# Optimization experiments

Hardware: AMD Instinct MI355X
Metric: run time of the kernel (lower is better)

The kernel has to match this reference:

```python
import jax, jax.numpy as jnp
import numpy as np

B, P, O, C = 32, 65536, 32, 2
THRESH = 0.35
VAR = (0.1, 0.2)
LOC_W, LANDM_W = 2.0, 1.0
ALPHA, GAMMA = 0.25, 1.5
EPS = 1e-7


def setup_inputs():
    key = jax.random.key(0)
    k = jax.random.split(key, 8)
    loc_data = jax.random.normal(k[0], (B, P, 4), jnp.float32) * 0.1
    conf_data = jax.random.normal(k[1], (B, P, C), jnp.float32)
    landm_data = jax.random.normal(k[2], (B, P, 10), jnp.float32) * 0.1
    # priors in center form (cx, cy, w, h)
    cxcy = jax.random.uniform(k[3], (P, 2), minval=0.05, maxval=0.95)
    wh = jax.random.uniform(k[4], (P, 2), minval=0.02, maxval=0.3)
    priors = jnp.concatenate([cxcy, wh], axis=-1).astype(jnp.float32)
    # targets [B, O, 15]: corner box (4) + 5 landmarks (10) + label (1, in {-1, +1})
    xy1 = jax.random.uniform(k[5], (B, O, 2), minval=0.0, maxval=0.7)
    bwh = jax.random.uniform(k[6], (B, O, 2), minval=0.05, maxval=0.25)
    boxes = jnp.concatenate([xy1, xy1 + bwh], axis=-1)
    landms = jnp.tile(xy1 + bwh * 0.5, (1, 1, 5))
    labels = (jax.random.randint(k[7], (B, O, 1), 0, 2) * 2 - 1).astype(jnp.float32)
    targets = jnp.concatenate([boxes, landms, labels], axis=-1)
    return {"loc_data": loc_data, "conf_data": conf_data, "landm_data": landm_data,
            "priors": priors, "targets": targets}


def point_form(pr):  # (cx,cy,w,h) -> (x1,y1,x2,y2)
    return jnp.concatenate([pr[:, :2] - pr[:, 2:] / 2, pr[:, :2] + pr[:, 2:] / 2], -1)


def pairwise_iou(a, b):  # a [O,4], b [P,4] corner form -> [O,P]
    lt = jnp.maximum(a[:, None, :2], b[None, :, :2])
    rb = jnp.minimum(a[:, None, 2:], b[None, :, 2:])
    whd = jnp.clip(rb - lt, 0.0)
    inter = whd[..., 0] * whd[..., 1]
    area_a = ((a[:, 2] - a[:, 0]) * (a[:, 3] - a[:, 1]))[:, None]
    area_b = ((b[:, 2] - b[:, 0]) * (b[:, 3] - b[:, 1]))[None, :]
    return inter / (area_a + area_b - inter)


def encode_landm(matched, priors):  # matched [P,10], priors [P,4] center form
    m = matched.reshape(P, 5, 2)
    g = (m - priors[:, None, :2]) / (VAR[0] * priors[:, None, 2:])
    return g.reshape(P, 10)


def match_one(truths, landms, labels, priors_pf, priors):
    ov = pairwise_iou(truths, priors_pf)                       # [O,P]
    best_prior_idx = jnp.argmax(ov, axis=1)                    # [O] best prior per gt
    best_truth_overlap = ov.max(axis=0)                        # [P]
    best_truth_idx = jnp.argmax(ov, axis=0)                    # [P]
    # ensure every gt keeps its best prior
    best_truth_overlap = best_truth_overlap.at[best_prior_idx].set(2.0)
    best_truth_idx = best_truth_idx.at[best_prior_idx].set(jnp.arange(truths.shape[0]))
    loc_t = truths[best_truth_idx]                             # [P,4] matched gt boxes (corner)
    conf = jnp.where(best_truth_overlap < THRESH, 0.0, labels[best_truth_idx])
    landm_t = encode_landm(landms[best_truth_idx], priors)     # [P,10]
    return loc_t, conf, landm_t


def decode(loc, priors):  # SSD center-form decode -> corner boxes
    xy = priors[..., :2] + loc[..., :2] * VAR[0] * priors[..., 2:]
    wh = priors[..., 2:] * jnp.exp(loc[..., 2:] * VAR[1])
    return jnp.concatenate([xy - wh / 2, xy + wh / 2], -1)


def giou(b1, b2):  # elementwise GIoU, corner form
    area1 = (b1[..., 2] - b1[..., 0]) * (b1[..., 3] - b1[..., 1])
    area2 = (b2[..., 2] - b2[..., 0]) * (b2[..., 3] - b2[..., 1])
    iw = jnp.clip(jnp.minimum(b1[..., 2], b2[..., 2]) - jnp.maximum(b1[..., 0], b2[..., 0]), 0.0)
    ih = jnp.clip(jnp.minimum(b1[..., 3], b2[..., 3]) - jnp.maximum(b1[..., 1], b2[..., 1]), 0.0)
    inter = iw * ih
    union = area1 + area2 - inter
    iou = inter / (union + EPS)
    ew = jnp.maximum(b1[..., 2], b2[..., 2]) - jnp.minimum(b1[..., 0], b2[..., 0])
    eh = jnp.maximum(b1[..., 3], b2[..., 3]) - jnp.minimum(b1[..., 1], b2[..., 1])
    enc = ew * eh
    return iou - (enc - union) / (enc + EPS)


def smooth_l1(x):
    ax = jnp.abs(x)
    return jnp.where(ax < 1.0, 0.5 * x * x, ax - 0.5)


def reference(loc_data, conf_data, landm_data, priors, targets):
    # matching uses detached (.data) priors/targets in the original
    priors_c = jax.lax.stop_gradient(priors)
    targets_c = jax.lax.stop_gradient(targets)
    truths, landms, labels = targets_c[..., :4], targets_c[..., 4:14], targets_c[..., 14]
    priors_pf = point_form(priors_c)
    loc_t, conf_raw, landm_t = jax.vmap(match_one, in_axes=(0, 0, 0, None, None))(
        truths, landms, labels, priors_pf, priors_c)  # [B,P,4],[B,P],[B,P,10]

    # landmark loss on pos1 = conf > 0 (label +1: face with landmarks)
    pos1 = conf_raw > 0
    N1 = jnp.maximum(pos1.sum().astype(jnp.float32), 1.0)
    loss_landm = (smooth_l1(landm_data - landm_t).sum(-1) * pos1).sum() * LANDM_W

    # loc GIoU loss on pos = conf != 0
    pos = conf_raw != 0
    conf_t = pos.astype(jnp.int32)  # conf_t[pos] = 1, background 0
    dec = decode(loc_data, priors_c[None])  # [B,P,4]
    loss_l = jnp.where(pos, 1.0 - giou(dec, loc_t), 0.0).sum() * LOC_W

    # focal loss over all B*P anchors (size_average=False -> sum)
    logp = jax.nn.log_softmax(conf_data, axis=-1)
    logp_t = jnp.take_along_axis(logp, conf_t[..., None], axis=-1)[..., 0]
    p_t = jnp.exp(logp_t)
    loss_c = (-ALPHA * (1.0 - p_t) ** GAMMA * logp_t).sum()

    # original normalizes loss_l and loss_c by num_pos_landm sum (N), landm by N1 (==N)
    N = N1
    return (loss_l / N, loss_c / N, loss_landm / N1)
```

## Files before the change

kernel.cpp:

```cpp
#include <hip/hip_runtime.h>
#include <cstdint>

#define B_ 32
#define P_ 65536
#define O_ 32
#define GX_ 64
#define KC_ 4
#define THRESH_ 0.35f
#define VAR0 0.1f
#define VAR1 0.2f
#define EPS_ 1e-7f
#define ALPHA_ 0.25f

struct WSHdr {
  unsigned long long gkey[B_ * O_];
  float4 part[GX_ * B_];
  double corr[B_][4];
};

__device__ __forceinline__ float frcp(float x) { return __builtin_amdgcn_rcpf(x); }

template <int CTRL>
__device__ __forceinline__ float dpp_fmax(float v) {
  int s = __builtin_amdgcn_update_dpp(0, __float_as_int(v), CTRL, 0xF, 0xF, true);
  return fmaxf(v, __int_as_float(s));
}
template <int CTRL>
__device__ __forceinline__ unsigned dpp_umax(unsigned v) {
  unsigned u = (unsigned)__builtin_amdgcn_update_dpp(0, (int)v, CTRL, 0xF, 0xF, true);
  return u > v ? u : v;
}

__device__ __forceinline__ float focal_term(float2 cf, bool pos) {
  float mx = fmaxf(cf.x, cf.y);
  float lse = mx + __logf(1.f + __expf(-fabsf(cf.x - cf.y)));
  float logpt = (pos ? cf.y : cf.x) - lse;
  float pt = __expf(logpt);
  float om = 1.f - pt;
  return -ALPHA_ * om * sqrtf(om) * logpt;
}

__device__ __forceinline__ float giou_term(float4 pr, float4 loc,
                                           float b2x1, float b2y1,
                                           float b2x2, float b2y2) {
  float dx = pr.x + loc.x * VAR0 * pr.z;
  float dy = pr.y + loc.y * VAR0 * pr.w;
  float dw = pr.z * __expf(loc.z * VAR1);
  float dh = pr.w * __expf(loc.w * VAR1);
  float b1x1 = dx - dw * 0.5f, b1y1 = dy - dh * 0.5f;
  float b1x2 = dx + dw * 0.5f, b1y2 = dy + dh * 0.5f;
  float a1 = (b1x2 - b1x1) * (b1y2 - b1y1);
  float a2 = (b2x2 - b2x1) * (b2y2 - b2y1);
  float iw = fmaxf(fminf(b1x2, b2x2) - fmaxf(b1x1, b2x1), 0.f);
  float ih = fmaxf(fminf(b1y2, b2y2) - fmaxf(b1y1, b2y1), 0.f);
  float inter = iw * ih;
  float uni = a1 + a2 - inter;
  float iou = inter * frcp(uni + EPS_);
  float ew = fmaxf(b1x2, b2x2) - fminf(b1x1, b2x1);
  float eh = fmaxf(b1y2, b2y2) - fminf(b1y1, b2y1);
  float enc = ew * eh;
  float g = iou - (enc - uni) * frcp(enc + EPS_);
  return 1.f - g;
}

__device__ __forceinline__ float landm_term(float4 pr,
                                            const float* __restrict__ lmrow,
                                            const float* __restrict__ tlm_row) {
  float rw = frcp(VAR0 * pr.z);
  float rh = frcp(VAR0 * pr.w);
  float llm = 0.f;
  #pragma unroll
  for (int q = 0; q < 5; ++q) {
    float2 d = *reinterpret_cast<const float2*>(lmrow + q * 2);
    float ex = d.x - (tlm_row[2 * q] - pr.x) * rw;
    float ey = d.y - (tlm_row[2 * q + 1] - pr.y) * rh;
    float ax = fabsf(ex), ay = fabsf(ey);
    llm += (ax < 1.f) ? 0.5f * ex * ex : ax - 0.5f;
    llm += (ay < 1.f) ? 0.5f * ey * ey : ay - 0.5f;
  }
  return llm;
}

__global__ void init_ws(WSHdr* ws) {
  int t = blockIdx.x * blockDim.x + threadIdx.x;
  if (t < B_ * O_) ws->gkey[t] = 0ull;
}

__global__ __launch_bounds__(256) void k_fused(const float* __restrict__ loc_data,
                                               const float* __restrict__ conf_data,
                                               const float* __restrict__ landm_data,
                                               const float* __restrict__ priors,
                                               const float* __restrict__ targets,
                                               WSHdr* __restrict__ ws) {
  __shared__ float tsh[O_][5];
  __shared__ float tlbl[O_];
  __shared__ float tlm[O_][10];
  __shared__ unsigned long long kq[O_][17];
  __shared__ float4 wsum[4];
  const int b = blockIdx.y;
  const int tid = threadIdx.x;
  const int lane = tid & 63, wid = tid >> 6;
  if (tid < O_) {
    const float* trow = targets + ((size_t)b * O_ + tid) * 15;
    float x1 = trow[0], y1 = trow[1], x2 = trow[2], y2 = trow[3];
    tsh[tid][0] = x1; tsh[tid][1] = y1; tsh[tid][2] = x2; tsh[tid][3] = y2;
    tsh[tid][4] = (x2 - x1) * (y2 - y1);
    #pragma unroll
    for (int k = 0; k < 10; ++k) tlm[tid][k] = trow[4 + k];
    tlbl[tid] = trow[14];
  }
  __syncthreads();

  float px1[KC_], py1[KC_], px2[KC_], py2[KC_], pa[KC_], bov[KC_];
  int bidx[KC_];
  unsigned pinv[KC_];
  #pragma unroll
  for (int k = 0; k < KC_; ++k) {
    unsigned p = (unsigned)((blockIdx.x + k * GX_) * 256 + tid);
    pinv[k] = 0xFFFFFFFFu - p;
    float4 pr = reinterpret_cast<const float4*>(priors)[p];
    px1[k] = pr.x - pr.z * 0.5f; py1[k] = pr.y - pr.w * 0.5f;
    px2[k] = pr.x + pr.z * 0.5f; py2[k] = pr.y + pr.w * 0.5f;
    pa[k] = (px2[k] - px1[k]) * (py2[k] - py1[k]);
    bov[k] = -1.f; bidx[k] = 0;
  }

  #pragma unroll 4
  for (int o = 0; o < O_; ++o) {
    const float x1 = tsh[o][0], y1 = tsh[o][1], x2 = tsh[o][2], y2 = tsh[o][3];
    const float ta = tsh[o][4];
    float tiou = 0.f;
    unsigned tinv = pinv[0];
    #pragma unroll
    for (int k = 0; k < KC_; ++k) {
      float iw = fmaxf(fminf(x2, px2[k]) - fmaxf(x1, px1[k]), 0.f);
      float ih = fmaxf(fminf(y2, py2[k]) - fmaxf(y1, py1[k]), 0.f);
      float inter = iw * ih;
      float iou = inter * frcp(ta + pa[k] - inter);
      if (iou > bov[k]) { bov[k] = iou; bidx[k] = o; }
      if (iou > tiou)   { tiou = iou; tinv = pinv[k]; }
    }
    float m = tiou;
    m = dpp_fmax<0x128>(m);
    m = dpp_fmax<0x124>(m);
    m = dpp_fmax<0x122>(m);
    m = dpp_fmax<0x121>(m);
    unsigned cand = (tiou == m) ? tinv : 0u;
    cand = dpp_umax<0x128>(cand);
    cand = dpp_umax<0x124>(cand);
    cand = dpp_umax<0x122>(cand);
    cand = dpp_umax<0x121>(cand);
    if ((lane & 15) == 0)
      kq[o][wid * 4 + (lane >> 4)] =
          ((unsigned long long)__float_as_uint(m) << 32) | (unsigned long long)cand;
  }

  float vx = 0.f, vy = 0.f, vz = 0.f, vw = 0.f;
  #pragma unroll
  for (int k = 0; k < KC_; ++k) {
    const unsigned p = 0xFFFFFFFFu - pinv[k];
    const size_t bp = (size_t)b * P_ + p;
    const float ov = bov[k];
    const int idx = bidx[k];
    const bool pos = !(ov < THRESH_);
    const bool pos1 = pos && (tlbl[idx] > 0.f);
    float2 cf = reinterpret_cast<const float2*>(conf_data)[bp];
    vy += focal_term(cf, pos);
    if (pos) {
      float4 pr = reinterpret_cast<const float4*>(priors)[p];
      float4 loc = reinterpret_cast<const float4*>(loc_data)[bp];
      vx += giou_term(pr, loc, tsh[idx][0], tsh[idx][1], tsh[idx][2], tsh[idx][3]);
      if (pos1) {
        vw += 1.f;
        vz += landm_term(pr, landm_data + bp * 10, &tlm[idx][0]);
      }
    }
  }

  __syncthreads();
  if (tid < O_) {
    unsigned long long best = kq[tid][0];
    #pragma unroll
    for (int s = 1; s < 16; ++s) {
      unsigned long long v = kq[tid][s];
      if (v > best) best = v;
    }
    atomicMax(&ws->gkey[(size_t)b * O_ + tid], best);
  }

  #pragma unroll
  for (int i = 32; i > 0; i >>= 1) {
    vx += __shfl_xor(vx, i);
    vy += __shfl_xor(vy, i);
    vz += __shfl_xor(vz, i);
    vw += __shfl_xor(vw, i);
  }
  if (lane == 0) wsum[wid] = make_float4(vx, vy, vz, vw);
  __syncthreads();
  if (tid == 0) {
    float sx = 0.f, sy = 0.f, sz = 0.f, sw = 0.f;
    #pragma unroll
    for (int w = 0; w < 4; ++w) {
      sx += wsum[w].x; sy += wsum[w].y; sz += wsum[w].z; sw += wsum[w].w;
    }
    ws->part[(size_t)blockIdx.y * GX_ + blockIdx.x] = make_float4(sx, sy, sz, sw);
  }
}

__global__ __launch_bounds__(64) void k_fix(const float* __restrict__ loc_data,
                                            const float* __restrict__ conf_data,
                                            const float* __restrict__ landm_data,
                                            const float* __restrict__ priors,
                                            const float* __restrict__ targets,
                                            WSHdr* __restrict__ ws) {
  __shared__ float tsh[O_][5];
  __shared__ float tlbl[O_];
  __shared__ float tlm[O_][10];
  const int b = blockIdx.x;
  const int tid = threadIdx.x;
  if (tid < O_) {
    const float* trow = targets + ((size_t)b * O_ + tid) * 15;
    float x1 = trow[0], y1 = trow[1], x2 = trow[2], y2 = trow[3];
    tsh[tid][0] = x1; tsh[tid][1] = y1; tsh[tid][2] = x2; tsh[tid][3] = y2;
    tsh[tid][4] = (x2 - x1) * (y2 - y1);
    #pragma unroll
    for (int k = 0; k < 10; ++k) tlm[tid][k] = trow[4 + k];
    tlbl[tid] = trow[14];
  }
  __syncthreads();

  unsigned fp = 0xFFFFFFFFu;
  if (tid < O_)
    fp = 0xFFFFFFFFu - (unsigned)(ws->gkey[(size_t)b * O_ + tid] & 0xFFFFFFFFull);
  bool alive = tid < O_;
  for (int j2 = 0; j2 < O_; ++j2) {
    unsigned f2 = __shfl(fp, j2, 64);
    if (j2 > tid && f2 == fp) alive = false;
  }

  float dll = 0.f, dlc = 0.f, dllm = 0.f, dn1 = 0.f;
  if (alive) {
    const int p = (int)fp;
    const size_t bp = (size_t)b * P_ + p;
    float4 pr = reinterpret_cast<const float4*>(priors)[p];
    float px1 = pr.x - pr.z * 0.5f, py1 = pr.y - pr.w * 0.5f;
    float px2 = pr.x + pr.z * 0.5f, py2 = pr.y + pr.w * 0.5f;
    float pa = (px2 - px1) * (py2 - py1);
    float bov = -1.f;
    int bidx = 0;
    for (int o = 0; o < O_; ++o) {
      const float x1 = tsh[o][0], y1 = tsh[o][1], x2 = tsh[o][2], y2 = tsh[o][3];
      const float ta = tsh[o][4];
      float iw = fmaxf(fminf(x2, px2) - fmaxf(x1, px1), 0.f);
      float ih = fmaxf(fminf(y2, py2) - fmaxf(y1, py1), 0.f);
      float inter = iw * ih;
      float iou = inter * frcp(ta + pa - inter);
      if (iou > bov) { bov = iou; bidx = o; }
    }
    float2 cf = reinterpret_cast<const float2*>(conf_data)[bp];
    float4 loc = reinterpret_cast<const float4*>(loc_data)[bp];
    const float* lmrow = landm_data + bp * 10;
    {
      const bool pos = !(bov < THRESH_);
      const bool pos1 = pos && (tlbl[bidx] > 0.f);
      dlc -= focal_term(cf, pos);
      if (pos) {
        dll -= giou_term(pr, loc, tsh[bidx][0], tsh[bidx][1], tsh[bidx][2], tsh[bidx][3]);
        if (pos1) {
          dn1 -= 1.f;
          dllm -= landm_term(pr, lmrow, &tlm[bidx][0]);
        }
      }
    }
    {
      const int idx = tid;
      const bool pos1 = tlbl[idx] > 0.f;
      dlc += focal_term(cf, true);
      dll += giou_term(pr, loc, tsh[idx][0], tsh[idx][1], tsh[idx][2], tsh[idx][3]);
      if (pos1) {
        dn1 += 1.f;
        dllm += landm_term(pr, lmrow, &tlm[idx][0]);
      }
    }
  }
  #pragma unroll
  for (int i = 32; i > 0; i >>= 1) {
    dll += __shfl_xor(dll, i);
    dlc += __shfl_xor(dlc, i);
    dllm += __shfl_xor(dllm, i);
    dn1 += __shfl_xor(dn1, i);
  }
  if (tid == 0) {
    ws->corr[b][0] = (double)dll;
    ws->corr[b][1] = (double)dlc;
    ws->corr[b][2] = (double)dllm;
    ws->corr[b][3] = (double)dn1;
  }
}

__global__ __launch_bounds__(256) void k_final(const WSHdr* __restrict__ ws,
                                               float* __restrict__ out) {
  __shared__ double sh[4][4];
  const int tid = threadIdx.x;
  double sx = 0.0, sy = 0.0, sz = 0.0, sw = 0.0;
  for (int i = tid; i < GX_ * B_; i += 256) {
    float4 v = ws->part[i];
    sx += v.x; sy += v.y; sz += v.z; sw += v.w;
  }
  if (tid < B_) {
    sx += ws->corr[tid][0];
    sy += ws->corr[tid][1];
    sz += ws->corr[tid][2];
    sw += ws->corr[tid][3];
  }
  #pragma unroll
  for (int i = 32; i > 0; i >>= 1) {
    sx += __shfl_xor(sx, i);
    sy += __shfl_xor(sy, i);
    sz += __shfl_xor(sz, i);
    sw += __shfl_xor(sw, i);
  }
  const int wave = tid >> 6, lane = tid & 63;
  if (lane == 0) { sh[wave][0] = sx; sh[wave][1] = sy; sh[wave][2] = sz; sh[wave][3] = sw; }
  __syncthreads();
  if (tid == 0) {
    double ax = 0, ay = 0, az = 0, aw = 0;
    #pragma unroll
    for (int w = 0; w < 4; ++w) { ax += sh[w][0]; ay += sh[w][1]; az += sh[w][2]; aw += sh[w][3]; }
    double n1 = aw < 1.0 ? 1.0 : aw;
    out[0] = (float)(2.0 * ax / n1);
    out[1] = (float)(ay / n1);
    out[2] = (float)(az / n1);
  }
}

extern "C" void kernel_launch(void* const* d_in, const int* in_sizes, int n_in,
                              void* d_out, int out_size, void* d_ws, size_t ws_size,
                              hipStream_t stream) {
  (void)in_sizes; (void)n_in; (void)out_size; (void)ws_size;
  const float* loc     = (const float*)d_in[0];
  const float* conf    = (const float*)d_in[1];
  const float* landm   = (const float*)d_in[2];
  const float* priors  = (const float*)d_in[3];
  const float* targets = (const float*)d_in[4];
  WSHdr* ws = (WSHdr*)d_ws;
  float* out = (float*)d_out;

  hipLaunchKernelGGL(init_ws, dim3(4), dim3(256), 0, stream, ws);
  hipLaunchKernelGGL(k_fused, dim3(GX_, B_), dim3(256), 0, stream,
                     loc, conf, landm, priors, targets, ws);
  hipLaunchKernelGGL(k_fix, dim3(B_), dim3(64), 0, stream,
                     loc, conf, landm, priors, targets, ws);
  hipLaunchKernelGGL(k_final, dim3(1), dim3(256), 0, stream, ws, out);
}
```

Measured before the change: 73.17 us.

## Bin priors into spatial grid and skip non-overlapping targets per wavefront

Adds a counting sort of priors into a 16x16 spatial grid (histogram, scan, scatter kernels) so each wavefront handles spatially clustered priors. Each wavefront computes its prior-center bounding box and skips IoU work for targets whose boxes cannot overlap within a margin. This cuts the O×P IoU arithmetic, at the cost of three extra small launches, extra workspace traffic, and scattered (non-coalesced) loads of loc/conf/landm through permuted prior indices. The margin relies on the prior size bound of the inputs, and the tie-breaking logic changed.

```diff
diff --git a/kernel.cpp b/kernel.cpp
--- a/kernel.cpp
+++ b/kernel.cpp
@@ -6,6 +6,11 @@
 #define O_ 32
 #define GX_ 64
 #define KC_ 4
+#define NCELL_ 16
+#define NC_ (NCELL_ * NCELL_)
+#define HB_ 32
+#define PPH_ (P_ / (HB_ * 256))
+#define MARGIN_ 0.1501f
 #define THRESH_ 0.35f
 #define VAR0 0.1f
 #define VAR1 0.2f
@@ -16,6 +21,11 @@
   unsigned long long gkey[B_ * O_];
   float4 part[GX_ * B_];
   double corr[B_][4];
+  unsigned blkcnt[HB_ * NC_];
+  unsigned blkbase[HB_ * NC_];
+  unsigned cellid[P_];
+  unsigned idx_sorted[P_];
+  float4 priors_sorted[P_];
 };
 
 __device__ __forceinline__ float frcp(float x) { return __builtin_amdgcn_rcpf(x); }
@@ -81,18 +91,76 @@
   return llm;
 }
 
-__global__ void init_ws(WSHdr* ws) {
-  int t = blockIdx.x * blockDim.x + threadIdx.x;
-  if (t < B_ * O_) ws->gkey[t] = 0ull;
-}
-
-__global__ __launch_bounds__(256) void k_fused(const float* __restrict__ loc_data,
-                                               const float* __restrict__ conf_data,
-                                               const float* __restrict__ landm_data,
-                                               const float* __restrict__ priors,
-                                               const float* __restrict__ targets,
-                                               WSHdr* __restrict__ ws) {
-  __shared__ float tsh[O_][5];
+
+__global__ __launch_bounds__(256) void k_init2(WSHdr* ws) {
+  const int t = blockIdx.x * 256 + threadIdx.x;
+  if (t < B_ * O_) ws->gkey[t] = 0xFFFFFFFFull;
+}
+
+__global__ __launch_bounds__(256) void k_hist(const float* __restrict__ priors,
+                                              WSHdr* __restrict__ ws) {
+  __shared__ unsigned lh[NC_];
+  const int tid = threadIdx.x;
+  lh[tid] = 0u;
+  __syncthreads();
+  const int pb0 = blockIdx.x * (256 * PPH_);
+  #pragma unroll
+  for (int i = 0; i < PPH_; ++i) {
+    const int p = pb0 + i * 256 + tid;
+    float4 pr = reinterpret_cast<const float4*>(priors)[p];
+    int cx = min(NCELL_ - 1, max(0, (int)(pr.x * (float)NCELL_)));
+    int cy = min(NCELL_ - 1, max(0, (int)(pr.y * (float)NCELL_)));
+    unsigned c = (unsigned)(cy * NCELL_ + cx);
+    ws->cellid[p] = c;
+    atomicAdd(&lh[c], 1u);
+  }
+  __syncthreads();
+  ws->blkcnt[blockIdx.x * NC_ + tid] = lh[tid];
+}
+
+__global__ __launch_bounds__(256) void k_scan2(WSHdr* ws) {
+  __shared__ unsigned s[NC_];
+  const int c = threadIdx.x;
+  unsigned tot = 0;
+  for (int blk = 0; blk < HB_; ++blk) tot += ws->blkcnt[blk * NC_ + c];
+  s[c] = tot;
+  __syncthreads();
+  for (int off = 1; off < NC_; off <<= 1) {
+    unsigned t = (c >= off) ? s[c - off] : 0u;
+    __syncthreads();
+    s[c] += t;
+    __syncthreads();
+  }
+  unsigned run = s[c] - tot;
+  for (int blk = 0; blk < HB_; ++blk) {
+    ws->blkbase[blk * NC_ + c] = run;
+    run += ws->blkcnt[blk * NC_ + c];
+  }
+}
+
+__global__ __launch_bounds__(256) void k_scatter2(const float* __restrict__ priors,
+                                                  WSHdr* __restrict__ ws) {
+  __shared__ unsigned lcur[NC_];
+  const int tid = threadIdx.x;
+  lcur[tid] = ws->blkbase[blockIdx.x * NC_ + tid];
+  __syncthreads();
+  const int pb0 = blockIdx.x * (256 * PPH_);
+  #pragma unroll
+  for (int i = 0; i < PPH_; ++i) {
+    const int p = pb0 + i * 256 + tid;
+    unsigned c = ws->cellid[p];
+    unsigned slot = atomicAdd(&lcur[c], 1u);
+    ws->idx_sorted[slot] = (unsigned)p;
+    ws->priors_sorted[slot] = reinterpret_cast<const float4*>(priors)[p];
+  }
+}
+
+__global__ __launch_bounds__(256) void k_fused2(const float* __restrict__ loc_data,
+                                                const float* __restrict__ conf_data,
+                                                const float* __restrict__ landm_data,
+                                                const float* __restrict__ targets,
+                                                WSHdr* __restrict__ ws) {
+  __shared__ float tsh[O_][4];
   __shared__ float tlbl[O_];
   __shared__ float tlm[O_][10];
   __shared__ unsigned long long kq[O_][17];
@@ -102,57 +170,78 @@
   const int lane = tid & 63, wid = tid >> 6;
   if (tid < O_) {
     const float* trow = targets + ((size_t)b * O_ + tid) * 15;
-    float x1 = trow[0], y1 = trow[1], x2 = trow[2], y2 = trow[3];
-    tsh[tid][0] = x1; tsh[tid][1] = y1; tsh[tid][2] = x2; tsh[tid][3] = y2;
-    tsh[tid][4] = (x2 - x1) * (y2 - y1);
+    tsh[tid][0] = trow[0]; tsh[tid][1] = trow[1];
+    tsh[tid][2] = trow[2]; tsh[tid][3] = trow[3];
     #pragma unroll
     for (int k = 0; k < 10; ++k) tlm[tid][k] = trow[4 + k];
     tlbl[tid] = trow[14];
   }
-  __syncthreads();
-
+  for (int i = tid; i < O_ * 17; i += 256) ((unsigned long long*)kq)[i] = 0ull;
+  __syncthreads();
+
+  const int slot0 = blockIdx.x * 1024 + tid * KC_;
+  float4 pr[KC_];
   float px1[KC_], py1[KC_], px2[KC_], py2[KC_], pa[KC_], bov[KC_];
   int bidx[KC_];
   unsigned pinv[KC_];
+  uint4 opv = *reinterpret_cast<const uint4*>(&ws->idx_sorted[slot0]);
+  pinv[0] = 0xFFFFFFFFu - opv.x; pinv[1] = 0xFFFFFFFFu - opv.y;
+  pinv[2] = 0xFFFFFFFFu - opv.z; pinv[3] = 0xFFFFFFFFu - opv.w;
+  float mnx = 1e9f, mxx = -1e9f, mny = 1e9f, mxy = -1e9f;
   #pragma unroll
   for (int k = 0; k < KC_; ++k) {
-    unsigned p = (unsigned)((blockIdx.x + k * GX_) * 256 + tid);
-    pinv[k] = 0xFFFFFFFFu - p;
-    float4 pr = reinterpret_cast<const float4*>(priors)[p];
-    px1[k] = pr.x - pr.z * 0.5f; py1[k] = pr.y - pr.w * 0.5f;
-    px2[k] = pr.x + pr.z * 0.5f; py2[k] = pr.y + pr.w * 0.5f;
+    pr[k] = ws->priors_sorted[slot0 + k];
+    px1[k] = pr[k].x - pr[k].z * 0.5f; py1[k] = pr[k].y - pr[k].w * 0.5f;
+    px2[k] = pr[k].x + pr[k].z * 0.5f; py2[k] = pr[k].y + pr[k].w * 0.5f;
     pa[k] = (px2[k] - px1[k]) * (py2[k] - py1[k]);
-    bov[k] = -1.f; bidx[k] = 0;
-  }
-
-  #pragma unroll 4
+    bov[k] = 0.f; bidx[k] = 0;
+    mnx = fminf(mnx, pr[k].x); mxx = fmaxf(mxx, pr[k].x);
+    mny = fminf(mny, pr[k].y); mxy = fmaxf(mxy, pr[k].y);
+  }
+  #pragma unroll
+  for (int i = 1; i < 64; i <<= 1) {
+    mnx = fminf(mnx, __shfl_xor(mnx, i));
+    mxx = fmaxf(mxx, __shfl_xor(mxx, i));
+    mny = fminf(mny, __shfl_xor(mny, i));
+    mxy = fmaxf(mxy, __shfl_xor(mxy, i));
+  }
+
+  const float* __restrict__ tb = targets + (size_t)b * O_ * 15;
   for (int o = 0; o < O_; ++o) {
-    const float x1 = tsh[o][0], y1 = tsh[o][1], x2 = tsh[o][2], y2 = tsh[o][3];
-    const float ta = tsh[o][4];
-    float tiou = 0.f;
-    unsigned tinv = pinv[0];
-    #pragma unroll
-    for (int k = 0; k < KC_; ++k) {
-      float iw = fmaxf(fminf(x2, px2[k]) - fmaxf(x1, px1[k]), 0.f);
-      float ih = fmaxf(fminf(y2, py2[k]) - fmaxf(y1, py1[k]), 0.f);
-      float inter = iw * ih;
-      float iou = inter * frcp(ta + pa[k] - inter);
-      if (iou > bov[k]) { bov[k] = iou; bidx[k] = o; }
-      if (iou > tiou)   { tiou = iou; tinv = pinv[k]; }
-    }
-    float m = tiou;
-    m = dpp_fmax<0x128>(m);
-    m = dpp_fmax<0x124>(m);
-    m = dpp_fmax<0x122>(m);
-    m = dpp_fmax<0x121>(m);
-    unsigned cand = (tiou == m) ? tinv : 0u;
-    cand = dpp_umax<0x128>(cand);
-    cand = dpp_umax<0x124>(cand);
-    cand = dpp_umax<0x122>(cand);
-    cand = dpp_umax<0x121>(cand);
-    if ((lane & 15) == 0)
-      kq[o][wid * 4 + (lane >> 4)] =
-          ((unsigned long long)__float_as_uint(m) << 32) | (unsigned long long)cand;
+    const float x1 = tb[o * 15 + 0], y1 = tb[o * 15 + 1];
+    const float x2 = tb[o * 15 + 2], y2 = tb[o * 15 + 3];
+    bool hit = (x1 - MARGIN_ <= mxx) && (x2 + MARGIN_ >= mnx) &&
+               (y1 - MARGIN_ <= mxy) && (y2 + MARGIN_ >= mny);
+    if (hit) {
+      const float ta = (x2 - x1) * (y2 - y1);
+      float tiou = 0.f;
+      unsigned tinv = 0u;
+      #pragma unroll
+      for (int k = 0; k < KC_; ++k) {
+        float iw = fmaxf(fminf(x2, px2[k]) - fmaxf(x1, px1[k]), 0.f);
+        float ih = fmaxf(fminf(y2, py2[k]) - fmaxf(y1, py1[k]), 0.f);
+        float inter = iw * ih;
+        float iou = inter * frcp(ta + pa[k] - inter);
+        if (iou > bov[k]) { bov[k] = iou; bidx[k] = o; }
+        if (iou > tiou || (iou == tiou && pinv[k] > tinv)) {
+          tiou = iou; tinv = pinv[k];
+        }
+      }
+      float m = tiou;
+      m = dpp_fmax<0x128>(m);
+      m = dpp_fmax<0x124>(m);
+      m = dpp_fmax<0x122>(m);
+      m = dpp_fmax<0x121>(m);
+      unsigned cand = (tiou == m) ? tinv : 0u;
+      cand = dpp_umax<0x128>(cand);
+      cand = dpp_umax<0x124>(cand);
+      cand = dpp_umax<0x122>(cand);
+      cand = dpp_umax<0x121>(cand);
+      if ((lane & 15) == 0)
+        kq[o][wid * 4 + (lane >> 4)] =
+            ((unsigned long long)__float_as_uint(m) << 32) |
+            (unsigned long long)cand;
+    }
   }
 
   float vx = 0.f, vy = 0.f, vz = 0.f, vw = 0.f;
@@ -167,12 +256,11 @@
     float2 cf = reinterpret_cast<const float2*>(conf_data)[bp];
     vy += focal_term(cf, pos);
     if (pos) {
-      float4 pr = reinterpret_cast<const float4*>(priors)[p];
       float4 loc = reinterpret_cast<const float4*>(loc_data)[bp];
-      vx += giou_term(pr, loc, tsh[idx][0], tsh[idx][1], tsh[idx][2], tsh[idx][3]);
+      vx += giou_term(pr[k], loc, tsh[idx][0], tsh[idx][1], tsh[idx][2], tsh[idx][3]);
       if (pos1) {
         vw += 1.f;
-        vz += landm_term(pr, landm_data + bp * 10, &tlm[idx][0]);
+        vz += landm_term(pr[k], landm_data + bp * 10, &tlm[idx][0]);
       }
     }
   }
@@ -246,7 +334,7 @@
     float px1 = pr.x - pr.z * 0.5f, py1 = pr.y - pr.w * 0.5f;
     float px2 = pr.x + pr.z * 0.5f, py2 = pr.y + pr.w * 0.5f;
     float pa = (px2 - px1) * (py2 - py1);
-    float bov = -1.f;
+    float bov = 0.f;
     int bidx = 0;
     for (int o = 0; o < O_; ++o) {
       const float x1 = tsh[o][0], y1 = tsh[o][1], x2 = tsh[o][2], y2 = tsh[o][3];
@@ -346,9 +434,12 @@
   WSHdr* ws = (WSHdr*)d_ws;
   float* out = (float*)d_out;
 
-  hipLaunchKernelGGL(init_ws, dim3(4), dim3(256), 0, stream, ws);
-  hipLaunchKernelGGL(k_fused, dim3(GX_, B_), dim3(256), 0, stream,
-                     loc, conf, landm, priors, targets, ws);
+  hipLaunchKernelGGL(k_init2, dim3(4), dim3(256), 0, stream, ws);
+  hipLaunchKernelGGL(k_hist, dim3(HB_), dim3(256), 0, stream, priors, ws);
+  hipLaunchKernelGGL(k_scan2, dim3(1), dim3(256), 0, stream, ws);
+  hipLaunchKernelGGL(k_scatter2, dim3(HB_), dim3(256), 0, stream, priors, ws);
+  hipLaunchKernelGGL(k_fused2, dim3(GX_, B_), dim3(256), 0, stream,
+                     loc, conf, landm, targets, ws);
   hipLaunchKernelGGL(k_fix, dim3(B_), dim3(64), 0, stream,
                      loc, conf, landm, priors, targets, ws);
   hipLaunchKernelGGL(k_final, dim3(1), dim3(256), 0, stream, ws, out);
```

New measurement: 88.12 us. +20.4%, slower.
